# Kernel tuning notes

Measured on AMD Instinct MI355X. Metric: run time of the kernel, lower is better.

Reference implementation:

```python
import jax, jax.numpy as jnp
import numpy as np

NUM_HASH_BUCKETS = 9311
OUT_CHANNELS = 64
B, C, L = 8192, 32, 8


def setup_inputs() -> dict:
    key = jax.random.key(0)
    k_x, k_emb = jax.random.split(key)
    x = jax.random.randint(k_x, (B, C, L), 0, NUM_HASH_BUCKETS, dtype=jnp.int64)
    emb_table = jax.random.normal(k_emb, (NUM_HASH_BUCKETS, OUT_CHANNELS), dtype=jnp.float32)
    # padding_idx=0 -> row 0 is zeros
    emb_table = emb_table.at[0].set(0.0)
    return {"x": x, "emb_table": emb_table}


def reference(x, emb_table):
    # x: [B, C, L] int64 category ids (0 = padding)
    num_buckets = emb_table.shape[0]
    x = jnp.maximum(x, 0)                      # relu (faithful to float branch; ints already >= 0)
    hashed = x % num_buckets                   # hash -> bucket id
    emb = emb_table[hashed]                    # gather: [B, C, L, D]
    mask = (x > 0).astype(emb.dtype)[..., None]  # [B, C, L, 1]
    sum_emb = jnp.sum(emb * mask, axis=2)      # [B, C, D]
    counts = jnp.maximum(jnp.sum(mask, axis=2), 1.0)  # [B, C, 1]
    return sum_emb / counts
```

## Files before the change

kernel.cpp:

```cpp
#include <hip/hip_runtime.h>


#define NPAIRS (8192 * 32)
#define LL 8
#define NROWS 9311
#define D 64
#define TAB_ELEMS (NROWS * D)

typedef float  vfloat4 __attribute__((ext_vector_type(4)));
typedef int    vint4   __attribute__((ext_vector_type(4)));
typedef unsigned int  uint32;
typedef unsigned int  vuint4 __attribute__((ext_vector_type(4)));
typedef unsigned short vushort4 __attribute__((ext_vector_type(4)));

__global__ __launch_bounds__(256) void
cvt_table_bf16(const vfloat4* __restrict__ src, vushort4* __restrict__ dst, int n4) {
    const int i = blockIdx.x * blockDim.x + threadIdx.x;
    if (i >= n4) return;
    const vfloat4 f = src[i];
    vushort4 o;
    #pragma unroll
    for (int k = 0; k < 4; ++k) {
        uint32 b = __float_as_uint(f[k]);
        b = (b + 0x7fff + ((b >> 16) & 1)) >> 16;
        o[k] = (unsigned short)b;
    }
    dst[i] = o;
}

__global__ __launch_bounds__(256) void
SharedMultiCategoricalEncoder_kernel(const int* __restrict__ x,
                                     const vuint4* __restrict__ tab,
                                     vfloat4* __restrict__ out4) {
    const int tid  = blockIdx.x * blockDim.x + threadIdx.x;
    const int pair = tid >> 3;
    const int sub  = tid & 7;

    const vint4* xp = (const vint4*)(x + pair * LL);
    const vint4 id01 = xp[0];
    const vint4 id23 = xp[1];
    const int ids[LL] = { id01.x, id01.y, id01.z, id01.w,
                          id23.x, id23.y, id23.z, id23.w };

    float acc[8] = {0.f};
    int cnt = 0;
#pragma unroll
    for (int l = 0; l < LL; ++l) {
        const int id = ids[l];
        const vuint4 e = tab[id * 8 + sub];
        #pragma unroll
        for (int k = 0; k < 4; ++k) {
            const uint32 u = e[k];
            acc[2*k]   += __uint_as_float(u << 16);
            acc[2*k+1] += __uint_as_float(u & 0xffff0000u);
        }
        cnt += (id > 0);
    }

    const float scale = 1.0f / (float)(cnt > 0 ? cnt : 1);
    vfloat4 lo = (vfloat4){acc[0], acc[1], acc[2], acc[3]} * scale;
    vfloat4 hi = (vfloat4){acc[4], acc[5], acc[6], acc[7]} * scale;

    vfloat4* op = out4 + pair * 16 + sub * 2;
    op[0] = lo;
    op[1] = hi;
}

extern "C" void kernel_launch(void* const* d_in, const int* in_sizes, int n_in,
                              void* d_out, int out_size, void* d_ws, size_t ws_size,
                              hipStream_t stream) {
    const int*   x   = (const int*)d_in[0];
    const float* emb = (const float*)d_in[1];
    float*       out = (float*)d_out;

    const int n4 = TAB_ELEMS / 4;
    cvt_table_bf16<<<(n4 + 255) / 256, 256, 0, stream>>>(
        (const vfloat4*)emb, (vushort4*)d_ws, n4);

    const int threads = 256;
    const int blocks  = (NPAIRS * 8) / threads;
    SharedMultiCategoricalEncoder_kernel<<<blocks, threads, 0, stream>>>(
        x, (const vuint4*)d_ws, (vfloat4*)out);
}
```

Baseline: 96.64 us.

## Process four pairs per thread with double-buffered table gathers

Each thread now handles four (batch, channel) pairs spaced a quarter of the problem apart, and the grid is four times smaller. Gathers for the next pair's eight rows are issued before the current pair's results are stored, keeping two sets of loads in flight per thread to raise memory-level parallelism. The cost is many more vector registers per thread (two 8x vuint4 buffers) and a quarter as many waves, which may lower occupancy and the latency hiding it provides.

```diff
diff --git a/kernel.cpp b/kernel.cpp
--- a/kernel.cpp
+++ b/kernel.cpp
@@ -6,6 +6,7 @@
 #define NROWS 9311
 #define D 64
 #define TAB_ELEMS (NROWS * D)
+#define QUARTER (NPAIRS / 4)
 
 typedef float  vfloat4 __attribute__((ext_vector_type(4)));
 typedef int    vint4   __attribute__((ext_vector_type(4)));
@@ -33,37 +34,59 @@
                                      const vuint4* __restrict__ tab,
                                      vfloat4* __restrict__ out4) {
     const int tid  = blockIdx.x * blockDim.x + threadIdx.x;
-    const int pair = tid >> 3;
+    const int base = tid >> 3;
     const int sub  = tid & 7;
+    const vint4* xp = (const vint4*)x;
 
-    const vint4* xp = (const vint4*)(x + pair * LL);
-    const vint4 id01 = xp[0];
-    const vint4 id23 = xp[1];
-    const int ids[LL] = { id01.x, id01.y, id01.z, id01.w,
-                          id23.x, id23.y, id23.z, id23.w };
-
-    float acc[8] = {0.f};
-    int cnt = 0;
+    vint4 ia[4], ib[4];
 #pragma unroll
-    for (int l = 0; l < LL; ++l) {
-        const int id = ids[l];
-        const vuint4 e = tab[id * 8 + sub];
-        #pragma unroll
-        for (int k = 0; k < 4; ++k) {
-            const uint32 u = e[k];
-            acc[2*k]   += __uint_as_float(u << 16);
-            acc[2*k+1] += __uint_as_float(u & 0xffff0000u);
-        }
-        cnt += (id > 0);
+    for (int k = 0; k < 4; ++k) {
+        const int p = base + k * QUARTER;
+        ia[k] = xp[2 * p];
+        ib[k] = xp[2 * p + 1];
     }
 
-    const float scale = 1.0f / (float)(cnt > 0 ? cnt : 1);
-    vfloat4 lo = (vfloat4){acc[0], acc[1], acc[2], acc[3]} * scale;
-    vfloat4 hi = (vfloat4){acc[4], acc[5], acc[6], acc[7]} * scale;
+    vuint4 e[2][8];
+#pragma unroll
+    for (int k = 0; k < 2; ++k) {
+        const int ids[LL] = { ia[k].x, ia[k].y, ia[k].z, ia[k].w,
+                              ib[k].x, ib[k].y, ib[k].z, ib[k].w };
+        #pragma unroll
+        for (int l = 0; l < LL; ++l) e[k][l] = tab[ids[l] * 8 + sub];
+    }
 
-    vfloat4* op = out4 + pair * 16 + sub * 2;
-    op[0] = lo;
-    op[1] = hi;
+#pragma unroll
+    for (int k = 0; k < 4; ++k) {
+        const int ids[LL] = { ia[k].x, ia[k].y, ia[k].z, ia[k].w,
+                              ib[k].x, ib[k].y, ib[k].z, ib[k].w };
+        int cnt = 0;
+        #pragma unroll
+        for (int l = 0; l < LL; ++l) cnt += (ids[l] > 0);
+
+        float acc[8] = {0.f};
+        #pragma unroll
+        for (int l = 0; l < LL; ++l) {
+            #pragma unroll
+            for (int q = 0; q < 4; ++q) {
+                const uint32 u = e[k & 1][l][q];
+                acc[2*q]   += __uint_as_float(u << 16);
+                acc[2*q+1] += __uint_as_float(u & 0xffff0000u);
+            }
+        }
+
+        if (k + 2 < 4) {
+            const int jds[LL] = { ia[k+2].x, ia[k+2].y, ia[k+2].z, ia[k+2].w,
+                                  ib[k+2].x, ib[k+2].y, ib[k+2].z, ib[k+2].w };
+            #pragma unroll
+            for (int l = 0; l < LL; ++l) e[k & 1][l] = tab[jds[l] * 8 + sub];
+        }
+
+        const float s = 1.0f / (float)(cnt > 0 ? cnt : 1);
+        const int p = base + k * QUARTER;
+        vfloat4* op = out4 + p * 16 + sub * 2;
+        op[0] = (vfloat4){acc[0], acc[1], acc[2], acc[3]} * s;
+        op[1] = (vfloat4){acc[4], acc[5], acc[6], acc[7]} * s;
+    }
 }
 
 extern "C" void kernel_launch(void* const* d_in, const int* in_sizes, int n_in,
@@ -78,7 +101,7 @@
         (const vfloat4*)emb, (vushort4*)d_ws, n4);
 
     const int threads = 256;
-    const int blocks  = (NPAIRS * 8) / threads;
+    const int blocks  = (QUARTER * 8) / threads;
     SharedMultiCategoricalEncoder_kernel<<<blocks, threads, 0, stream>>>(
         x, (const vuint4*)d_ws, (vfloat4*)out);
 }
```

After: 92.03 us. -4.8%, faster.
